# Performance work log

Hardware: AMD Instinct MI355X
Metric: run time of the kernel (lower is better)

Reference implementation:

```python
import jax, jax.numpy as jnp
import numpy as np

NUM_HEADS = 2  # embed_dim=8 fixed by n_wires=8 in QLayer

def setup_inputs() -> dict:
    key = jax.random.key(0)
    k1, k2, k3 = jax.random.split(key, 3)
    x = jax.random.normal(k1, (32, 2048, 8), dtype=jnp.float32)
    theta = jax.random.normal(k2, (8,), dtype=jnp.float32)       # trainable RX angles
    W_out = jax.random.normal(k3, (8, 8), dtype=jnp.float32) * 0.35  # out_proj weight (no bias)
    return {"x": x, "theta": theta, "W_out": W_out}

def reference(x, theta, W_out):
    B, S, E = x.shape
    H = NUM_HEADS
    d_k = E // H
    # Quantum layer: RX(x_i) then RX(theta_i) on wire i from |0>, measure PauliZ
    # => <Z_i> = cos(x_i + theta_i). k = q = v = this (three identical calls on x).
    h = jnp.cos(x + theta)                                  # [B, S, E]
    h = h.reshape(B, S, H, d_k).transpose(0, 2, 1, 3)        # [B, H, S, d_k]
    scale = 1.0 / jnp.sqrt(jnp.asarray(d_k, dtype=h.dtype))
    scores = jnp.einsum('bhqd,bhkd->bhqk', h, h) * scale     # [B, H, S, S]
    attn = jax.nn.softmax(scores, axis=-1)                   # dropout: eval-mode identity
    out = jnp.einsum('bhqk,bhkd->bhqd', attn, h)             # [B, H, S, d_k]
    out = out.transpose(0, 2, 1, 3).reshape(B, S, E)         # merge heads
    return out @ W_out.T                                     # nn.Linear(E, E, bias=False)
```

## Files before the change

kernel.cpp:

```cpp
#include <hip/hip_runtime.h>

#define NB 32
#define NS 2048
#define QS 0.72134752044448170367f

typedef _Float16 f16;
typedef _Float16 h2 __attribute__((ext_vector_type(2)));
typedef _Float16 h4 __attribute__((ext_vector_type(4)));
typedef _Float16 h8 __attribute__((ext_vector_type(8)));
typedef float f32x4 __attribute__((ext_vector_type(4)));

__device__ __forceinline__ h2 cvt_pk_f16(float a, float b) {
  return __builtin_bit_cast(h2, __builtin_amdgcn_cvt_pkrtz(a, b));
}

#define TR_STRIDE 1032
#define TR_BASE 8192
#define LDS_HALVES (8192 + 10 * 1032)
#define ZIDX (TR_BASE + 9 * TR_STRIDE)

__global__ __launch_bounds__(512, 4) void attn_fused_kernel(
    const float* __restrict__ x, const float* __restrict__ theta,
    const float* __restrict__ Wout, float* __restrict__ outp) {
  __shared__ __align__(16) f16 lds[LDS_HALVES];

  const int b = blockIdx.y;
  const int t = threadIdx.x;
  const int w = t >> 6;
  const int lane = t & 63;
  const int g = lane >> 4;
  const int n = lane & 15;

  float th[8];
#pragma unroll
  for (int e = 0; e < 8; ++e) th[e] = theta[e];

#pragma unroll
  for (int i = 0; i < 2; ++i) {
    const int l = t + 512 * i;
    const float4* xr = (const float4*)(x + ((size_t)b * NS + l) * 8);
    float4 lo = xr[0], hi = xr[1];
    h8 hv;
    hv[0] = (f16)__cosf(lo.x + th[0]);
    hv[1] = (f16)__cosf(lo.y + th[1]);
    hv[2] = (f16)__cosf(lo.z + th[2]);
    hv[3] = (f16)__cosf(lo.w + th[3]);
    hv[4] = (f16)__cosf(hi.x + th[4]);
    hv[5] = (f16)__cosf(hi.y + th[5]);
    hv[6] = (f16)__cosf(hi.z + th[6]);
    hv[7] = (f16)__cosf(hi.w + th[7]);
    ((h8*)lds)[l] = hv;
#pragma unroll
    for (int e = 0; e < 8; ++e) lds[TR_BASE + e * TR_STRIDE + l] = hv[e];
    lds[TR_BASE + 8 * TR_STRIDE + l] = (f16)1.0f;
    lds[ZIDX + l] = (f16)0.0f;
  }

  float4 pf[2][2];
#pragma unroll
  for (int i = 0; i < 2; ++i) {
    const int l = t + 512 * i;
    const float4* xr = (const float4*)(x + ((size_t)b * NS + 1024 + l) * 8);
    pf[i][0] = xr[0];
    pf[i][1] = xr[1];
  }

  h8 Bq0, Bq1;
#pragma unroll
  for (int j = 0; j < 8; ++j) {
    Bq0[j] = (f16)0.f;
    Bq1[j] = (f16)0.f;
  }
  if (g == 0) {
    const float4* xq = (const float4*)(
        x + ((size_t)b * NS + blockIdx.x * 128 + w * 16 + n) * 8);
    float4 lo = xq[0], hi = xq[1];
    Bq0[0] = (f16)(__cosf(lo.x + th[0]) * QS);
    Bq0[1] = (f16)(__cosf(lo.y + th[1]) * QS);
    Bq0[2] = (f16)(__cosf(lo.z + th[2]) * QS);
    Bq0[3] = (f16)(__cosf(lo.w + th[3]) * QS);
    Bq1[0] = (f16)(__cosf(hi.x + th[4]) * QS);
    Bq1[1] = (f16)(__cosf(hi.y + th[5]) * QS);
    Bq1[2] = (f16)(__cosf(hi.z + th[6]) * QS);
    Bq1[3] = (f16)(__cosf(hi.w + th[7]) * QS);
  }

  const int sini = (g == 0) ? n * 8 : ZIDX;
  const int sadv = (g == 0) ? 256 : 0;

  const int d0 = (n < 4) ? n : ((n == 4) ? 8 : 9);
  const int d1 = (n < 4) ? (n + 4) : d0;
  const int t0ini = TR_BASE + d0 * TR_STRIDE + 4 * g;
  const int t1ini = TR_BASE + d1 * TR_STRIDE + 4 * g;

  const f32x4 Z = {0.f, 0.f, 0.f, 0.f};
  f32x4 C0 = Z;
  f32x4 C1 = Z;

  __syncthreads();

  for (int chunk = 0; chunk < 2; ++chunk) {
    if (chunk == 1) {
      __syncthreads();
#pragma unroll
      for (int i = 0; i < 2; ++i) {
        const int l = t + 512 * i;
        float4 lo = pf[i][0], hi = pf[i][1];
        h8 hv;
        hv[0] = (f16)__cosf(lo.x + th[0]);
        hv[1] = (f16)__cosf(lo.y + th[1]);
        hv[2] = (f16)__cosf(lo.z + th[2]);
        hv[3] = (f16)__cosf(lo.w + th[3]);
        hv[4] = (f16)__cosf(hi.x + th[4]);
        hv[5] = (f16)__cosf(hi.y + th[5]);
        hv[6] = (f16)__cosf(hi.z + th[6]);
        hv[7] = (f16)__cosf(hi.w + th[7]);
        ((h8*)lds)[l] = hv;
#pragma unroll
        for (int e = 0; e < 8; ++e) lds[TR_BASE + e * TR_STRIDE + l] = hv[e];
      }
      __syncthreads();
    }

    int sc = sini;
    int tc0 = t0ini;
    int tc1 = t1ini;
#pragma unroll 2
    for (int step = 0; step < 32; ++step) {
      h4 k00 = *(const h4*)(lds + sc);
      h4 k10 = *(const h4*)(lds + sc + 4);
      h4 k01 = *(const h4*)(lds + sc + 128);
      h4 k11 = *(const h4*)(lds + sc + 132);
      h4 a00 = *(const h4*)(lds + tc0);
      h4 a01 = *(const h4*)(lds + tc0 + 16);
      h4 a10 = *(const h4*)(lds + tc1);
      h4 a11 = *(const h4*)(lds + tc1 + 16);

      h8 A00, A01, A10, A11, V0, V1;
#pragma unroll
      for (int j = 0; j < 4; ++j) {
        A00[j] = k00[j];
        A01[j] = k01[j];
        A10[j] = k10[j];
        A11[j] = k11[j];
        A00[j + 4] = (f16)0.f;
        A01[j + 4] = (f16)0.f;
        A10[j + 4] = (f16)0.f;
        A11[j + 4] = (f16)0.f;
        V0[j] = a00[j];
        V0[j + 4] = a01[j];
        V1[j] = a10[j];
        V1[j + 4] = a11[j];
      }

      f32x4 S00 = __builtin_amdgcn_mfma_f32_16x16x32_f16(A00, Bq0, Z, 0, 0, 0);
      f32x4 S01 = __builtin_amdgcn_mfma_f32_16x16x32_f16(A01, Bq0, Z, 0, 0, 0);
      f32x4 S10 = __builtin_amdgcn_mfma_f32_16x16x32_f16(A10, Bq1, Z, 0, 0, 0);
      f32x4 S11 = __builtin_amdgcn_mfma_f32_16x16x32_f16(A11, Bq1, Z, 0, 0, 0);

      h8 B0, B1;
      h2 p;
      p = cvt_pk_f16(__builtin_amdgcn_exp2f(S00[0]),
                     __builtin_amdgcn_exp2f(S00[1]));
      B0[0] = p[0];
      B0[1] = p[1];
      p = cvt_pk_f16(__builtin_amdgcn_exp2f(S00[2]),
                     __builtin_amdgcn_exp2f(S00[3]));
      B0[2] = p[0];
      B0[3] = p[1];
      p = cvt_pk_f16(__builtin_amdgcn_exp2f(S01[0]),
                     __builtin_amdgcn_exp2f(S01[1]));
      B0[4] = p[0];
      B0[5] = p[1];
      p = cvt_pk_f16(__builtin_amdgcn_exp2f(S01[2]),
                     __builtin_amdgcn_exp2f(S01[3]));
      B0[6] = p[0];
      B0[7] = p[1];
      p = cvt_pk_f16(__builtin_amdgcn_exp2f(S10[0]),
                     __builtin_amdgcn_exp2f(S10[1]));
      B1[0] = p[0];
      B1[1] = p[1];
      p = cvt_pk_f16(__builtin_amdgcn_exp2f(S10[2]),
                     __builtin_amdgcn_exp2f(S10[3]));
      B1[2] = p[0];
      B1[3] = p[1];
      p = cvt_pk_f16(__builtin_amdgcn_exp2f(S11[0]),
                     __builtin_amdgcn_exp2f(S11[1]));
      B1[4] = p[0];
      B1[5] = p[1];
      p = cvt_pk_f16(__builtin_amdgcn_exp2f(S11[2]),
                     __builtin_amdgcn_exp2f(S11[3]));
      B1[6] = p[0];
      B1[7] = p[1];

      C0 = __builtin_amdgcn_mfma_f32_16x16x32_f16(V0, B0, C0, 0, 0, 0);
      C1 = __builtin_amdgcn_mfma_f32_16x16x32_f16(V1, B1, C1, 0, 0, 0);

      sc += sadv;
      tc0 += 32;
      tc1 += 32;
    }
  }

  const float den0 = __shfl(C0[0], 16 + n, 64);
  const float den1 = __shfl(C1[0], 16 + n, 64);
  if (lane < 16) {
    const float i0 = 1.0f / den0, i1 = 1.0f / den1;
    float m8[8] = {C0[0] * i0, C0[1] * i0, C0[2] * i0, C0[3] * i0,
                   C1[0] * i1, C1[1] * i1, C1[2] * i1, C1[3] * i1};
    float o[8];
#pragma unroll
    for (int e = 0; e < 8; ++e) {
      float s = 0.f;
#pragma unroll
      for (int f = 0; f < 8; ++f) s += m8[f] * Wout[e * 8 + f];
      o[e] = s;
    }
    const int q = blockIdx.x * 128 + w * 16 + n;
    float4* op = (float4*)(outp + ((size_t)b * NS + q) * 8);
    op[0] = make_float4(o[0], o[1], o[2], o[3]);
    op[1] = make_float4(o[4], o[5], o[6], o[7]);
  }
}

extern "C" void kernel_launch(void* const* d_in, const int* in_sizes, int n_in,
                              void* d_out, int out_size, void* d_ws,
                              size_t ws_size, hipStream_t stream) {
  const float* x = (const float*)d_in[0];
  const float* theta = (const float*)d_in[1];
  const float* W = (const float*)d_in[2];
  float* out = (float*)d_out;
  (void)d_ws;
  (void)ws_size;

  attn_fused_kernel<<<dim3(NS / 128, NB), 512, 0, stream>>>(x, theta, W, out);
}
```

Before: 92.71 us.

## Split key range across wave pairs and halve queries per block

Each block now handles 64 queries, and two waves share each 16-query tile, each processing half the keys of every chunk. The partial numerator and denominator accumulators are reduced through LDS before normalization and the output projection. The grid doubles and the launch bound asks for higher occupancy, aiming to shorten the serial MFMA/exp chain per wave. The cost is that each block redundantly recomputes the full key cosine table in LDS, doubling that prologue work across the grid, plus an extra reduction sync.

```diff
diff --git a/kernel.cpp b/kernel.cpp
--- a/kernel.cpp
+++ b/kernel.cpp
@@ -19,7 +19,7 @@
 #define LDS_HALVES (8192 + 10 * 1032)
 #define ZIDX (TR_BASE + 9 * TR_STRIDE)
 
-__global__ __launch_bounds__(512, 4) void attn_fused_kernel(
+__global__ __launch_bounds__(512, 8) void attn_fused_kernel(
     const float* __restrict__ x, const float* __restrict__ theta,
     const float* __restrict__ Wout, float* __restrict__ outp) {
   __shared__ __align__(16) f16 lds[LDS_HALVES];
@@ -30,6 +30,8 @@
   const int lane = t & 63;
   const int g = lane >> 4;
   const int n = lane & 15;
+  const int qt = w & 3;
+  const int h = w >> 2;
 
   float th[8];
 #pragma unroll
@@ -73,7 +75,7 @@
   }
   if (g == 0) {
     const float4* xq = (const float4*)(
-        x + ((size_t)b * NS + blockIdx.x * 128 + w * 16 + n) * 8);
+        x + ((size_t)b * NS + blockIdx.x * 64 + qt * 16 + n) * 8);
     float4 lo = xq[0], hi = xq[1];
     Bq0[0] = (f16)(__cosf(lo.x + th[0]) * QS);
     Bq0[1] = (f16)(__cosf(lo.y + th[1]) * QS);
@@ -85,13 +87,13 @@
     Bq1[3] = (f16)(__cosf(hi.w + th[7]) * QS);
   }
 
-  const int sini = (g == 0) ? n * 8 : ZIDX;
+  const int sini = (g == 0) ? (h * 512 + n) * 8 : ZIDX;
   const int sadv = (g == 0) ? 256 : 0;
 
   const int d0 = (n < 4) ? n : ((n == 4) ? 8 : 9);
   const int d1 = (n < 4) ? (n + 4) : d0;
-  const int t0ini = TR_BASE + d0 * TR_STRIDE + 4 * g;
-  const int t1ini = TR_BASE + d1 * TR_STRIDE + 4 * g;
+  const int t0ini = TR_BASE + d0 * TR_STRIDE + h * 512 + 4 * g;
+  const int t1ini = TR_BASE + d1 * TR_STRIDE + h * 512 + 4 * g;
 
   const f32x4 Z = {0.f, 0.f, 0.f, 0.f};
   f32x4 C0 = Z;
@@ -126,7 +128,7 @@
     int tc0 = t0ini;
     int tc1 = t1ini;
 #pragma unroll 2
-    for (int step = 0; step < 32; ++step) {
+    for (int step = 0; step < 16; ++step) {
       h4 k00 = *(const h4*)(lds + sc);
       h4 k10 = *(const h4*)(lds + sc + 4);
       h4 k01 = *(const h4*)(lds + sc + 128);
@@ -202,24 +204,50 @@
     }
   }
 
-  const float den0 = __shfl(C0[0], 16 + n, 64);
-  const float den1 = __shfl(C1[0], 16 + n, 64);
-  if (lane < 16) {
-    const float i0 = 1.0f / den0, i1 = 1.0f / den1;
-    float m8[8] = {C0[0] * i0, C0[1] * i0, C0[2] * i0, C0[3] * i0,
-                   C1[0] * i1, C1[1] * i1, C1[2] * i1, C1[3] * i1};
-    float o[8];
-#pragma unroll
-    for (int e = 0; e < 8; ++e) {
-      float s = 0.f;
-#pragma unroll
-      for (int f = 0; f < 8; ++f) s += m8[f] * Wout[e * 8 + f];
-      o[e] = s;
+  __syncthreads();
+  float* kvf = (float*)lds;
+  if (h == 1) {
+    float* mb = kvf + ((size_t)(qt * 64 + lane)) * 9;
+    mb[0] = C0[0];
+    mb[1] = C0[1];
+    mb[2] = C0[2];
+    mb[3] = C0[3];
+    mb[4] = C1[0];
+    mb[5] = C1[1];
+    mb[6] = C1[2];
+    mb[7] = C1[3];
+  }
+  __syncthreads();
+  if (h == 0) {
+    const float* mb = kvf + ((size_t)(qt * 64 + lane)) * 9;
+    C0[0] += mb[0];
+    C0[1] += mb[1];
+    C0[2] += mb[2];
+    C0[3] += mb[3];
+    C1[0] += mb[4];
+    C1[1] += mb[5];
+    C1[2] += mb[6];
+    C1[3] += mb[7];
+
+    const float den0 = __shfl(C0[0], 16 + n, 64);
+    const float den1 = __shfl(C1[0], 16 + n, 64);
+    if (lane < 16) {
+      const float i0 = 1.0f / den0, i1 = 1.0f / den1;
+      float m8[8] = {C0[0] * i0, C0[1] * i0, C0[2] * i0, C0[3] * i0,
+                     C1[0] * i1, C1[1] * i1, C1[2] * i1, C1[3] * i1};
+      float o[8];
+#pragma unroll
+      for (int e = 0; e < 8; ++e) {
+        float s = 0.f;
+#pragma unroll
+        for (int f = 0; f < 8; ++f) s += m8[f] * Wout[e * 8 + f];
+        o[e] = s;
+      }
+      const int q = blockIdx.x * 64 + qt * 16 + n;
+      float4* op = (float4*)(outp + ((size_t)b * NS + q) * 8);
+      op[0] = make_float4(o[0], o[1], o[2], o[3]);
+      op[1] = make_float4(o[4], o[5], o[6], o[7]);
     }
-    const int q = blockIdx.x * 128 + w * 16 + n;
-    float4* op = (float4*)(outp + ((size_t)b * NS + q) * 8);
-    op[0] = make_float4(o[0], o[1], o[2], o[3]);
-    op[1] = make_float4(o[4], o[5], o[6], o[7]);
   }
 }
 
@@ -233,5 +261,5 @@
   (void)d_ws;
   (void)ws_size;
 
-  attn_fused_kernel<<<dim3(NS / 128, NB), 512, 0, stream>>>(x, theta, W, out);
+  attn_fused_kernel<<<dim3(NS / 64, NB), 512, 0, stream>>>(x, theta, W, out);
 }
```

New measurement: 96.94 us. +4.6%, slower.
